# Performance work log

Measured on AMD Instinct MI355X. Metric: run time of the kernel, lower is better.

## Reference

```python
import jax, jax.numpy as jnp
import numpy as np

TEMPERATURE = 0.5  # sampler_config['temperature']
EPS = jnp.float32(np.finfo(np.float32).tiny)  # torch.finfo(float32).tiny


def setup_inputs() -> dict:
    key = jax.random.key(0)
    # att: [B graphs, N nodes per graph, M = Gnum_m subgraph samples]
    att = jax.random.normal(key, (256, 1024, 4), dtype=jnp.float32)
    return {"att": att, "k": 128}


def _continuous_topk(att, k, noise_key):
    """Iterative Gumbel-softmax relaxed top-k (Sampler.sample_subset +
    Sampler.continuous_topk with separate=False), batched over graphs (B)
    and subgraph samples (M).

    att: [B, N, M] node attention logits per graph per sample.
    Returns khot: [B, N, M], sum of k relaxed one-hot selections.
    """
    # gumbel_keys: z = -log(-log(U + eps))
    u = jax.random.uniform(noise_key, att.shape, dtype=att.dtype)
    att_g = att - jnp.log(-jnp.log(u + EPS))

    state0 = (att_g, jnp.zeros_like(att_g), jnp.zeros_like(att_g))

    def step(state, _):
        ag, onehot, khot = state
        khot_mask = jnp.maximum(1.0 - onehot, EPS)
        ag = ag + jnp.log(khot_mask)
        # softmax over the node axis (dim 0 of each per-graph slice in the original)
        onehot = jax.nn.softmax(ag / TEMPERATURE, axis=1)
        return (ag, onehot, khot + onehot), None

    (_, _, khot), _ = jax.lax.scan(step, state0, None, length=k)
    return khot


def reference(att, k):
    # Relaxed k-hot selection scores; the original then argsorts these per
    # graph to pick the top-k node indices (non-differentiable bookkeeping).
    return _continuous_topk(att, k, jax.random.key(42))
```

## Files before the change

kernel.cpp:

```cpp
#include <hip/hip_runtime.h>
#include <math.h>


#define N_NODES 1024

typedef float f2 __attribute__((ext_vector_type(2)));

__device__ __forceinline__ unsigned rotl32(unsigned x, int r) {
  return (x << r) | (x >> (32 - r));
}

__device__ __forceinline__ void threefry2x32(unsigned k0, unsigned k1,
                                             unsigned& x0, unsigned& x1) {
  const unsigned ks0 = k0, ks1 = k1, ks2 = k0 ^ k1 ^ 0x1BD11BDAu;
  x0 += ks0; x1 += ks1;
  x0 += x1; x1 = rotl32(x1, 13); x1 ^= x0;
  x0 += x1; x1 = rotl32(x1, 15); x1 ^= x0;
  x0 += x1; x1 = rotl32(x1, 26); x1 ^= x0;
  x0 += x1; x1 = rotl32(x1, 6);  x1 ^= x0;
  x0 += ks1; x1 += ks2 + 1u;
  x0 += x1; x1 = rotl32(x1, 17); x1 ^= x0;
  x0 += x1; x1 = rotl32(x1, 29); x1 ^= x0;
  x0 += x1; x1 = rotl32(x1, 16); x1 ^= x0;
  x0 += x1; x1 = rotl32(x1, 24); x1 ^= x0;
  x0 += ks2; x1 += ks0 + 2u;
  x0 += x1; x1 = rotl32(x1, 13); x1 ^= x0;
  x0 += x1; x1 = rotl32(x1, 15); x1 ^= x0;
  x0 += x1; x1 = rotl32(x1, 26); x1 ^= x0;
  x0 += x1; x1 = rotl32(x1, 6);  x1 ^= x0;
  x0 += ks0; x1 += ks1 + 3u;
  x0 += x1; x1 = rotl32(x1, 17); x1 ^= x0;
  x0 += x1; x1 = rotl32(x1, 29); x1 ^= x0;
  x0 += x1; x1 = rotl32(x1, 16); x1 ^= x0;
  x0 += x1; x1 = rotl32(x1, 24); x1 ^= x0;
  x0 += ks1; x1 += ks2 + 4u;
  x0 += x1; x1 = rotl32(x1, 13); x1 ^= x0;
  x0 += x1; x1 = rotl32(x1, 15); x1 ^= x0;
  x0 += x1; x1 = rotl32(x1, 26); x1 ^= x0;
  x0 += x1; x1 = rotl32(x1, 6);  x1 ^= x0;
  x0 += ks2; x1 += ks0 + 5u;
}

template <int CTRL>
__device__ __forceinline__ float dpp_sum_step(float v) {
  int t = __builtin_amdgcn_update_dpp(0, __float_as_int(v), CTRL, 0xf, 0xf, true);
  return v + __int_as_float(t);
}
template <int CTRL>
__device__ __forceinline__ float dpp_max_step(float v) {
  int iv = __float_as_int(v);
  int t = __builtin_amdgcn_update_dpp(iv, iv, CTRL, 0xf, 0xf, false);
  return fmaxf(v, __int_as_float(t));
}

__device__ __forceinline__ float wave_sum64(float v) {
  v = dpp_sum_step<0x111>(v);
  v = dpp_sum_step<0x112>(v);
  v = dpp_sum_step<0x114>(v);
  v = dpp_sum_step<0x118>(v);
  v = dpp_sum_step<0x142>(v);
  v = dpp_sum_step<0x143>(v);
  return __int_as_float(__builtin_amdgcn_readlane(__float_as_int(v), 63));
}
__device__ __forceinline__ float wave_max64(float v) {
  v = dpp_max_step<0x111>(v);
  v = dpp_max_step<0x112>(v);
  v = dpp_max_step<0x114>(v);
  v = dpp_max_step<0x118>(v);
  v = dpp_max_step<0x142>(v);
  v = dpp_max_step<0x143>(v);
  return __int_as_float(__builtin_amdgcn_readlane(__float_as_int(v), 63));
}

__global__ __launch_bounds__(64)
void Sampler_72619307040792_kernel(const float* __restrict__ att,
                                   const int* __restrict__ kp,
                                   float* __restrict__ out) {
  const int col = blockIdx.x;
  const int b = col >> 2;
  const int m = col & 3;
  const int lane = threadIdx.x;
  const int k = *kp;

  const float EPS = __uint_as_float(0x00800000u);
  const int base = b * 4096 + m;

  float g[16];
  f2 w[8], kh[8];

#pragma unroll
  for (int j = 0; j < 16; ++j) {
    const int n = j * 64 + lane;
    const unsigned idx = (unsigned)(base + n * 4);
    unsigned c0 = 0u, c1 = idx;
    threefry2x32(0u, 42u, c0, c1);
    const unsigned bits = c0 ^ c1;
    const float u = __uint_as_float((bits >> 9) | 0x3F800000u) - 1.0f;
    const float gum = -logf(-logf(u + EPS));
    g[j] = 2.0f * (att[idx] + gum);
  }

  float mx = g[0];
#pragma unroll
  for (int j = 1; j < 16; ++j) mx = fmaxf(mx, g[j]);
  mx = wave_max64(mx);

#pragma unroll
  for (int p = 0; p < 8; ++p) {
    f2 t;
    t.x = expf(g[2 * p] - mx);
    t.y = expf(g[2 * p + 1] - mx);
    w[p] = t;
    kh[p] = (f2)(0.0f);
  }

  const f2 one = (f2)(1.0f);
  for (int it = 0; it < k; ++it) {
    f2 s0 = w[0] + w[1];
    f2 s1 = w[2] + w[3];
    f2 s2 = w[4] + w[5];
    f2 s3 = w[6] + w[7];
    f2 sA = s0 + s1;
    f2 sB = s2 + s3;
    f2 sC = sA + sB;
    float sv = sC.x + sC.y;
    const float S = wave_sum64(sv);
    const float rinv = __builtin_amdgcn_rcpf(S);
    f2 rv;
    rv.x = rinv;
    rv.y = rinv;
#pragma unroll
    for (int p = 0; p < 8; ++p)
      kh[p] = __builtin_elementwise_fma(w[p], rv, kh[p]);
#pragma unroll
    for (int p = 0; p < 8; ++p) {
      const f2 u = __builtin_elementwise_fma(-w[p], rv, one);
      const f2 t = w[p] * u;
      w[p] = t * u;
    }
  }

#pragma unroll
  for (int p = 0; p < 8; ++p) {
    out[base + (2 * p * 64 + lane) * 4] = kh[p].x;
    out[base + ((2 * p + 1) * 64 + lane) * 4] = kh[p].y;
  }
}

extern "C" void kernel_launch(void* const* d_in, const int* in_sizes, int n_in,
                              void* d_out, int out_size, void* d_ws, size_t ws_size,
                              hipStream_t stream) {
  const float* att = (const float*)d_in[0];
  const int* kp = (const int*)d_in[1];
  float* out = (float*)d_out;
  const int cols = out_size / N_NODES;
  Sampler_72619307040792_kernel<<<cols, 64, 0, stream>>>(att, kp, out);
}
```

Baseline: 32.19 us.

## Update softmax normalizer via power-sum recurrence to decouple wave reductions

After a few direct iterations, the kernel computes the next normalizer S algebraically from sums of w^2 and w^3 instead of re-reducing the updated weights. The two wave reductions for those power sums are independent and can overlap, moving the reduction off the serial dependency on S. This adds extra per-lane multiply work and risks numerical drift from cancellation in the recurrence. Launch bounds are also set to one block per CU hint.

```diff
diff --git a/kernel.cpp b/kernel.cpp
--- a/kernel.cpp
+++ b/kernel.cpp
@@ -3,6 +3,7 @@
 
 
 #define N_NODES 1024
+#define HEAD 4
 
 typedef float f2 __attribute__((ext_vector_type(2)));
 
@@ -72,7 +73,18 @@
   return __int_as_float(__builtin_amdgcn_readlane(__float_as_int(v), 63));
 }
 
-__global__ __launch_bounds__(64)
+__device__ __forceinline__ float lane_tree8(const f2* a) {
+  f2 s0 = a[0] + a[1];
+  f2 s1 = a[2] + a[3];
+  f2 s2 = a[4] + a[5];
+  f2 s3 = a[6] + a[7];
+  f2 sA = s0 + s1;
+  f2 sB = s2 + s3;
+  f2 sC = sA + sB;
+  return sC.x + sC.y;
+}
+
+__global__ __launch_bounds__(64, 1)
 void Sampler_72619307040792_kernel(const float* __restrict__ att,
                                    const int* __restrict__ kp,
                                    float* __restrict__ out) {
@@ -115,20 +127,16 @@
   }
 
   const f2 one = (f2)(1.0f);
-  for (int it = 0; it < k; ++it) {
-    f2 s0 = w[0] + w[1];
-    f2 s1 = w[2] + w[3];
-    f2 s2 = w[4] + w[5];
-    f2 s3 = w[6] + w[7];
-    f2 sA = s0 + s1;
-    f2 sB = s2 + s3;
-    f2 sC = sA + sB;
-    float sv = sC.x + sC.y;
-    const float S = wave_sum64(sv);
-    const float rinv = __builtin_amdgcn_rcpf(S);
+  float S, r;
+
+  int it = 0;
+  const int head = (k < HEAD) ? k : HEAD;
+  for (; it < head; ++it) {
+    S = wave_sum64(lane_tree8(w));
+    r = __builtin_amdgcn_rcpf(S);
     f2 rv;
-    rv.x = rinv;
-    rv.y = rinv;
+    rv.x = r;
+    rv.y = r;
 #pragma unroll
     for (int p = 0; p < 8; ++p)
       kh[p] = __builtin_elementwise_fma(w[p], rv, kh[p]);
@@ -137,6 +145,57 @@
       const f2 u = __builtin_elementwise_fma(-w[p], rv, one);
       const f2 t = w[p] * u;
       w[p] = t * u;
+    }
+  }
+
+  if (it < k) {
+    S = wave_sum64(lane_tree8(w));
+    r = __builtin_amdgcn_rcpf(S);
+    f2 w2[8];
+#pragma unroll
+    for (int p = 0; p < 8; ++p) w2[p] = w[p] * w[p];
+    float tp = lane_tree8(w2);
+    f2 qa = (f2)(0.0f), qb = (f2)(0.0f);
+#pragma unroll
+    for (int p = 0; p < 8; p += 2) {
+      qa = __builtin_elementwise_fma(w2[p], w[p], qa);
+      qb = __builtin_elementwise_fma(w2[p + 1], w[p + 1], qb);
+    }
+    {
+      const f2 qs = qa + qb;
+      float tq = qs.x + qs.y;
+
+      for (; it < k; ++it) {
+        const float P = wave_sum64(tp);
+        const float Q = wave_sum64(tq);
+        f2 rv;
+        rv.x = r;
+        rv.y = r;
+#pragma unroll
+        for (int p = 0; p < 8; ++p)
+          kh[p] = __builtin_elementwise_fma(w[p], rv, kh[p]);
+#pragma unroll
+        for (int p = 0; p < 8; ++p) {
+          const f2 u = __builtin_elementwise_fma(-w[p], rv, one);
+          const f2 t = w[p] * u;
+          w[p] = t * u;
+        }
+#pragma unroll
+        for (int p = 0; p < 8; ++p) w2[p] = w[p] * w[p];
+        tp = lane_tree8(w2);
+        qa = (f2)(0.0f);
+        qb = (f2)(0.0f);
+#pragma unroll
+        for (int p = 0; p < 8; p += 2) {
+          qa = __builtin_elementwise_fma(w2[p], w[p], qa);
+          qb = __builtin_elementwise_fma(w2[p + 1], w[p + 1], qb);
+        }
+        const f2 qs2 = qa + qb;
+        tq = qs2.x + qs2.y;
+        const float c1 = fmaf(-2.0f * r, P, S);
+        S = fmaf(r * r, Q, c1);
+        r = __builtin_amdgcn_rcpf(S);
+      }
     }
   }
 
```

Result: slower. 39.19 us (+21.7%).
